# Kernel tuning notes

Hardware: AMD Instinct MI355X
Metric: run time of the kernel (lower is better)

## Reference

```python
import jax, jax.numpy as jnp
import numpy as np

N = 20000      # nodes
E = 160000     # edges
F_IN = 128     # num_node_features
D = 128        # embedding_size (out_channels)
H = 4          # heads
NEG = 0.2      # GATv2Conv negative_slope
N_LAYERS = 3


def setup_inputs() -> dict:
    key = jax.random.key(0)
    ks = jax.random.split(key, 12)
    s = 0.05
    return {
        "x": jax.random.normal(ks[0], (N, F_IN), jnp.float32),
        "edge_index": jax.random.randint(ks[1], (2, E), 0, N, jnp.int64),
        "edge_attr": jax.random.normal(ks[2], (E, 2), jnp.float32),
        "Wf": jax.random.normal(ks[3], (F_IN, D), jnp.float32) * s,
        "bf": jnp.zeros((D,), jnp.float32),
        "Wl": jax.random.normal(ks[4], (D, H * D), jnp.float32) * s,
        "bl": jnp.zeros((H * D,), jnp.float32),
        "Wr": jax.random.normal(ks[5], (D, H * D), jnp.float32) * s,
        "br": jnp.zeros((H * D,), jnp.float32),
        "We": jax.random.normal(ks[6], (2, H * D), jnp.float32) * s,
        "att": jax.random.normal(ks[7], (H, D), jnp.float32) * s,
        "bias_out": jnp.zeros((D,), jnp.float32),
    }


def reference(x, edge_index, edge_attr, Wf, bf, Wl, bl, Wr, br, We, att, bias_out):
    src, dst = edge_index[0], edge_index[1]

    # add_self_loops with fill_value='mean': self-loop edge_attr = mean of
    # incoming edge_attr per node (0 where a node has no incoming edges)
    ea_sum = jax.ops.segment_sum(edge_attr, dst, num_segments=N)            # [N,2]
    cnt = jax.ops.segment_sum(jnp.ones((E,), edge_attr.dtype), dst, num_segments=N)
    loop_attr = ea_sum / jnp.maximum(cnt, 1.0)[:, None]
    loop_idx = jnp.arange(N, dtype=src.dtype)
    fsrc = jnp.concatenate([src, loop_idx])                                  # [E+N]
    fdst = jnp.concatenate([dst, loop_idx])
    fea = jnp.concatenate([edge_attr, loop_attr], axis=0)                    # [E+N,2]

    ee = (fea @ We).reshape(-1, H, D)                                        # [E+N,H,D]

    def gatv2_layer(h):
        xl = (h @ Wl + bl).reshape(N, H, D)   # lin_l -> source-side / message
        xr = (h @ Wr + br).reshape(N, H, D)   # lin_r -> target-side
        e = jax.nn.leaky_relu(xl[fsrc] + xr[fdst] + ee, NEG)                 # [E+N,H,D]
        logits = jnp.einsum('ehd,hd->eh', e, att)                            # [E+N,H]
        m = jax.ops.segment_max(logits, fdst, num_segments=N)                # [N,H]
        w = jnp.exp(logits - m[fdst])
        denom = jax.ops.segment_sum(w, fdst, num_segments=N)                 # [N,H]
        alpha = w / denom[fdst]                                              # segment softmax
        msg = xl[fsrc] * alpha[..., None]                                    # [E+N,H,D]
        out = jax.ops.segment_sum(msg, fdst, num_segments=N)                 # [N,H,D]
        return out.mean(axis=1) + bias_out                                   # concat=False

    h = x @ Wf + bf
    for _ in range(N_LAYERS):
        h = jax.nn.leaky_relu(gatv2_layer(h), 0.01)  # F.leaky_relu default slope
    return h
```

## Files before the change

kernel.cpp:

```cpp
#include <hip/hip_runtime.h>
#include <hip/hip_bf16.h>

#define NN 20000
#define NE 160000
#define EF (NE + NN)
#define DD 128
#define HH 4
#define NPA (NN * DD)
#define NPW (1024 * 128 + 128 * 128 + 1024)
#define DEGB ((NE + 255) / 256)
#define NBLK 40

typedef unsigned short u16;
typedef unsigned int u32;

using short8  = __attribute__((ext_vector_type(8))) short;
using ushort8 = __attribute__((ext_vector_type(8))) unsigned short;
using float4v = __attribute__((ext_vector_type(4))) float;

__device__ __forceinline__ float bf2f(u16 u) {
    union { u32 i; float f; } c;
    c.i = ((u32)u) << 16;
    return c.f;
}
__device__ __forceinline__ u16 f2bf(float f) {
    union { float f; u32 u; } c;
    c.f = f;
    u32 u = c.u;
    u32 r = (u + 0x7fffu + ((u >> 16) & 1u)) >> 16;
    return (u16)r;
}


__global__ void k_zero_i(int* __restrict__ p, int n) {
    int i = blockIdx.x * blockDim.x + threadIdx.x;
    if (i < n) p[i] = 0;
}

__global__ void k_zero_f(float* __restrict__ p, int n) {
    int i = blockIdx.x * blockDim.x + threadIdx.x;
    if (i < n) p[i] = 0.f;
}


__global__ void k_degpack(const int* __restrict__ ei, const float* __restrict__ ea,
                          const float* __restrict__ x,
                          const float* __restrict__ Wl, const float* __restrict__ Wr,
                          const float* __restrict__ bl, const float* __restrict__ br,
                          const float* __restrict__ Wf,
                          int* __restrict__ cnt, float* __restrict__ ea_sum,
                          u16* __restrict__ Axh, u16* __restrict__ Axl,
                          u16* __restrict__ W2Th, u16* __restrict__ W2Tl,
                          u16* __restrict__ WfTh, u16* __restrict__ WfTl,
                          float* __restrict__ bias2) {
    int gb = blockIdx.x;
    if (gb < DEGB) {
        int e = gb * 256 + threadIdx.x;
        if (e >= NE) return;
        int t = ei[NE + e];
        atomicAdd(&cnt[t], 1);
        atomicAdd(&ea_sum[t * 2 + 0], ea[e * 2 + 0]);
        atomicAdd(&ea_sum[t * 2 + 1], ea[e * 2 + 1]);
        return;
    }
    int i = (gb - DEGB) * 256 + threadIdx.x;
    if (i < NPA) {
        float a = x[i];
        u16 h = f2bf(a);
        Axh[i] = h;
        Axl[i] = f2bf(a - bf2f(h));
        return;
    }
    i -= NPA;
    if (i < 1024 * 128) {
        int n = i >> 7, k = i & 127;
        float w = (n < 512) ? Wl[k * 512 + n] : Wr[k * 512 + (n - 512)];
        u16 h = f2bf(w);
        W2Th[n * 128 + k] = h;
        W2Tl[n * 128 + k] = f2bf(w - bf2f(h));
    } else if (i < 1024 * 128 + 128 * 128) {
        int u = i - 1024 * 128;
        int n = u >> 7, k = u & 127;
        float w = Wf[k * 128 + n];
        u16 h = f2bf(w);
        WfTh[n * 128 + k] = h;
        WfTl[n * 128 + k] = f2bf(w - bf2f(h));
    } else if (i < NPW) {
        int n = i - (1024 * 128 + 128 * 128);
        bias2[n] = (n < 512) ? bl[n] : br[n - 512];
    }
}


__global__ __launch_bounds__(512) void k_scan_a(const int* __restrict__ cnt,
                                                int* __restrict__ rowptr,
                                                int* __restrict__ bsum) {
    __shared__ int ws[8];
    int tid = threadIdx.x;
    int i = blockIdx.x * 512 + tid;
    int l = tid & 63, w = tid >> 6;
    int v = (i < NN) ? (cnt[i] + 1) : 0;
    #pragma unroll
    for (int off = 1; off < 64; off <<= 1) {
        int u = __shfl_up(v, off, 64);
        if (l >= off) v += u;
    }
    if (l == 63) ws[w] = v;
    __syncthreads();
    if (w == 0) {
        int s = (l < 8) ? ws[l] : 0;
        #pragma unroll
        for (int off = 1; off < 8; off <<= 1) {
            int u = __shfl_up(s, off, 64);
            if (l >= off) s += u;
        }
        if (l < 8) ws[l] = s;
    }
    __syncthreads();
    v += (w > 0) ? ws[w - 1] : 0;
    if (i < NN) rowptr[i + 1] = v;
    if (tid == 511) bsum[blockIdx.x] = v;
}

__global__ void k_scan_c(int* __restrict__ rowptr, const int* __restrict__ bsum) {
    int l = threadIdx.x & 63;
    int v = (l < NBLK) ? bsum[l] : 0;
    #pragma unroll
    for (int off = 1; off < 64; off <<= 1) {
        int u = __shfl_up(v, off, 64);
        if (l >= off) v += u;
    }
    int i = blockIdx.x * blockDim.x + threadIdx.x;
    int j = i >> 9;
    int off = (j > 0) ? __shfl(v, j - 1, 64) : 0;
    if (i < NN) rowptr[i + 1] += off;
    if (i == 0) rowptr[0] = 0;
}


__global__ void k_fill(const int* __restrict__ ei, const float* __restrict__ ea,
                       const int* __restrict__ rowptr, int* __restrict__ fillc,
                       const int* __restrict__ cnt, const float* __restrict__ ea_sum,
                       int* __restrict__ srcs,
                       float* __restrict__ fa0, float* __restrict__ fa1) {
    int e = blockIdx.x * blockDim.x + threadIdx.x;
    if (e < NE) {
        int s = ei[e], t = ei[NE + e];
        int pos = atomicAdd(&fillc[t], 1);
        int slot = rowptr[t] + pos;
        srcs[slot] = s;
        fa0[slot] = ea[e * 2];
        fa1[slot] = ea[e * 2 + 1];
    } else if (e < NE + NN) {
        int n = e - NE;
        int slot = rowptr[n + 1] - 1;
        srcs[slot] = n;
        float c = fmaxf((float)cnt[n], 1.f);
        fa0[slot] = ea_sum[n * 2 + 0] / c;
        fa1[slot] = ea_sum[n * 2 + 1] / c;
    }
}


template<int SPLIT, int NB>
__global__ __launch_bounds__(256, 3) void k_mgemm(
        const u16* __restrict__ Ahg, const u16* __restrict__ Alg,
        const u16* __restrict__ BTh, const u16* __restrict__ BTl,
        const float* __restrict__ bias, float* __restrict__ C1,
        u16* __restrict__ C2b,
        u16* __restrict__ Oh, u16* __restrict__ Ol, int M) {
    __shared__ u16 sAh[64 * 128], sBh[64 * 128], sBl[64 * 128];
    int m0 = blockIdx.y * 64;
    int t = threadIdx.x;
    int lane = t & 63;
    int wm = (t >> 6) & 1;
    int wn = t >> 7;
    int fm = lane & 15;
    int q8 = (lane >> 4) * 8;

    short8 fal[4][2];
    #pragma unroll
    for (int i = 0; i < 2; ++i) {
        const u16* p = Alg + (size_t)(m0 + wm * 32 + i * 16 + fm) * 128 + q8;
        #pragma unroll
        for (int kk = 0; kk < 4; ++kk)
            fal[kk][i] = *(const short8*)(p + kk * 32);
    }

    #pragma unroll
    for (int i = 0; i < 4; ++i) {
        int c = t + 256 * i;
        int row = c >> 4, ch = c & 15;
        int gm = m0 + row;
        short8 va = {0, 0, 0, 0, 0, 0, 0, 0};
        if (gm < M) va = *(const short8*)&Ahg[gm * 128 + ch * 8];
        *(short8*)&sAh[row * 128 + ((ch ^ (row & 15)) << 3)] = va;
    }

    int cq = q8 >> 3;

    for (int bb = 0; bb < NB; ++bb) {
        int n0 = (blockIdx.x * NB + bb) * 64;
        __syncthreads();
        #pragma unroll
        for (int i = 0; i < 4; ++i) {
            int c = t + 256 * i;
            int row = c >> 4, ch = c & 15;
            int gn = n0 + row;
            int d = row * 128 + ((ch ^ (row & 15)) << 3);
            *(short8*)&sBh[d] = *(const short8*)&BTh[gn * 128 + ch * 8];
            *(short8*)&sBl[d] = *(const short8*)&BTl[gn * 128 + ch * 8];
        }
        __syncthreads();

        float4v zz = {0.f, 0.f, 0.f, 0.f};
        float4v acc[2][2];
        acc[0][0] = zz; acc[0][1] = zz; acc[1][0] = zz; acc[1][1] = zz;

        #pragma unroll
        for (int k0 = 0; k0 < 128; k0 += 32) {
            int cl = (k0 >> 3) + cq;
            int sw = (cl ^ fm) << 3;
            short8 fah[2], fbh[2], fbl[2];
            #pragma unroll
            for (int i = 0; i < 2; ++i) {
                int mr = wm * 32 + i * 16 + fm;
                fah[i] = *(const short8*)&sAh[mr * 128 + sw];
                int nr = wn * 32 + i * 16 + fm;
                fbh[i] = *(const short8*)&sBh[nr * 128 + sw];
                fbl[i] = *(const short8*)&sBl[nr * 128 + sw];
            }
            #pragma unroll
            for (int i = 0; i < 2; ++i)
                #pragma unroll
                for (int j = 0; j < 2; ++j) {
                    acc[i][j] = __builtin_amdgcn_mfma_f32_16x16x32_bf16(fah[i], fbh[j], acc[i][j], 0, 0, 0);
                    acc[i][j] = __builtin_amdgcn_mfma_f32_16x16x32_bf16(fah[i], fbl[j], acc[i][j], 0, 0, 0);
                    acc[i][j] = __builtin_amdgcn_mfma_f32_16x16x32_bf16(fal[k0 >> 5][i], fbh[j], acc[i][j], 0, 0, 0);
                }
        }

        #pragma unroll
        for (int i = 0; i < 2; ++i) {
            #pragma unroll
            for (int j = 0; j < 2; ++j) {
                int gn = n0 + wn * 32 + j * 16 + fm;
                float bv = bias[gn];
                #pragma unroll
                for (int r = 0; r < 4; ++r) {
                    int gm = m0 + wm * 32 + i * 16 + (lane >> 4) * 4 + r;
                    if (gm < M) {
                        float v = acc[i][j][r] + bv;
                        if (SPLIT) {
                            u16 h = f2bf(v);
                            Oh[gm * 128 + gn] = h;
                            Ol[gm * 128 + gn] = f2bf(v - bf2f(h));
                        } else if (n0 < 512) {
                            C1[gm * 512 + gn] = v;
                        } else {
                            C2b[gm * 512 + gn - 512] = f2bf(v);
                        }
                    }
                }
            }
        }
    }
}


__global__ __launch_bounds__(256) void k_gat(
        const int* __restrict__ rowptr, const int* __restrict__ srcs,
        const float* __restrict__ fa0, const float* __restrict__ fa1,
        const float* __restrict__ xl, const u16* __restrict__ xr,
        const float* __restrict__ We, const float* __restrict__ att,
        const float* __restrict__ bias_out,
        u16* __restrict__ Oh, u16* __restrict__ Ol,
        float* __restrict__ outp, int last) {
    __shared__ float sacc[2][512];
    __shared__ float sden[2][4];
    int wv = threadIdx.x >> 6;
    int pair = wv >> 1;
    int half = wv & 1;
    int n = blockIdx.x * 2 + pair;
    int l = threadIdx.x & 63;
    int d0 = l * 8;
    float xrv[8], we0[8], we1[8], atv[8];
    {
        ushort8 u = *reinterpret_cast<const ushort8*>(&xr[(size_t)n * 512 + d0]);
        #pragma unroll
        for (int k = 0; k < 8; ++k) xrv[k] = bf2f(u[k]);
        float4 a = *reinterpret_cast<const float4*>(&We[d0]);
        float4 b = *reinterpret_cast<const float4*>(&We[d0 + 4]);
        we0[0]=a.x; we0[1]=a.y; we0[2]=a.z; we0[3]=a.w;
        we0[4]=b.x; we0[5]=b.y; we0[6]=b.z; we0[7]=b.w;
        a = *reinterpret_cast<const float4*>(&We[512 + d0]);
        b = *reinterpret_cast<const float4*>(&We[512 + d0 + 4]);
        we1[0]=a.x; we1[1]=a.y; we1[2]=a.z; we1[3]=a.w;
        we1[4]=b.x; we1[5]=b.y; we1[6]=b.z; we1[7]=b.w;
        a = *reinterpret_cast<const float4*>(&att[d0]);
        b = *reinterpret_cast<const float4*>(&att[d0 + 4]);
        atv[0]=a.x; atv[1]=a.y; atv[2]=a.z; atv[3]=a.w;
        atv[4]=b.x; atv[5]=b.y; atv[6]=b.z; atv[7]=b.w;
    }
    int b0 = rowptr[n], b1 = rowptr[n + 1];
    float acc[8] = {0.f,0.f,0.f,0.f,0.f,0.f,0.f,0.f};
    float den = 0.f;
    int e0 = b0 + half;
    if (e0 < b1) {
        int sNext = srcs[e0];
        for (int e = e0; e < b1; e += 2) {
            int s = sNext;
            if (e + 2 < b1) sNext = srcs[e + 2];
            float f0 = fa0[e], f1 = fa1[e];
            const float* xlp = &xl[(size_t)s * 512 + d0];
            float4 a = *reinterpret_cast<const float4*>(xlp);
            float4 b = *reinterpret_cast<const float4*>(xlp + 4);
            float xv[8] = {a.x, a.y, a.z, a.w, b.x, b.y, b.z, b.w};
            float p = 0.f;
            #pragma unroll
            for (int k = 0; k < 8; ++k) {
                float v = xv[k] + xrv[k] + f0 * we0[k] + f1 * we1[k];
                v = v > 0.f ? v : 0.2f * v;
                p += v * atv[k];
            }
            p += __shfl_xor(p, 1, 64);
            p += __shfl_xor(p, 2, 64);
            p += __shfl_xor(p, 4, 64);
            p += __shfl_xor(p, 8, 64);
            float wt = __expf(p);
            den += wt;
            #pragma unroll
            for (int k = 0; k < 8; ++k) acc[k] += wt * xv[k];
        }
    }
    if (half == 1) {
        *reinterpret_cast<float4*>(&sacc[pair][d0]) =
            make_float4(acc[0], acc[1], acc[2], acc[3]);
        *reinterpret_cast<float4*>(&sacc[pair][d0 + 4]) =
            make_float4(acc[4], acc[5], acc[6], acc[7]);
        if ((l & 15) == 0) sden[pair][l >> 4] = den;
    }
    __syncthreads();
    if (half == 1) return;
    #pragma unroll
    for (int k = 0; k < 8; ++k) acc[k] += sacc[pair][d0 + k];
    den += sden[pair][l >> 4];
    float inv = 1.f / den;
    float val[8];
    #pragma unroll
    for (int k = 0; k < 8; ++k) {
        float v = acc[k] * inv;
        v += __shfl_xor(v, 16, 64);
        v += __shfl_xor(v, 32, 64);
        val[k] = v;
    }
    if (l < 16) {
        #pragma unroll
        for (int k = 0; k < 8; ++k) {
            float v = val[k] * 0.25f + bias_out[d0 + k];
            v = v > 0.f ? v : 0.01f * v;
            val[k] = v;
        }
        if (last) {
            #pragma unroll
            for (int k = 0; k < 8; ++k) outp[n * 128 + d0 + k] = val[k];
        } else {
            #pragma unroll
            for (int k = 0; k < 8; ++k) {
                u16 hv = f2bf(val[k]);
                Oh[n * 128 + d0 + k] = hv;
                Ol[n * 128 + d0 + k] = f2bf(val[k] - bf2f(hv));
            }
        }
    }
}


extern "C" void kernel_launch(void* const* d_in, const int* in_sizes, int n_in,
                              void* d_out, int out_size, void* d_ws, size_t ws_size,
                              hipStream_t stream) {
    size_t o = 0;
    auto alloc = [&](size_t bytes) { size_t cur = o; o += (bytes + 255) & ~(size_t)255; return cur; };
    size_t off_cnt    = alloc((size_t)NN * 4);
    size_t off_fillc  = alloc((size_t)NN * 4);
    size_t off_easum  = alloc((size_t)NN * 2 * 4);
    size_t off_rowptr = alloc((size_t)(NN + 1) * 4);
    size_t off_bsum   = alloc((size_t)NBLK * 4);
    size_t off_srcs   = alloc((size_t)EF * 4);
    size_t off_fa0    = alloc((size_t)EF * 4);
    size_t off_fa1    = alloc((size_t)EF * 4);
    size_t off_axh    = alloc((size_t)NN * DD * 2);
    size_t off_axl    = alloc((size_t)NN * DD * 2);
    size_t off_ah     = alloc((size_t)NN * DD * 2);
    size_t off_al     = alloc((size_t)NN * DD * 2);
    size_t off_xl     = alloc((size_t)NN * 512 * 4);
    size_t off_xr     = alloc((size_t)NN * 512 * 2);
    size_t off_w2th   = alloc((size_t)1024 * 128 * 2);
    size_t off_w2tl   = alloc((size_t)1024 * 128 * 2);
    size_t off_wfth   = alloc((size_t)128 * 128 * 2);
    size_t off_wftl   = alloc((size_t)128 * 128 * 2);
    size_t off_bias2  = alloc((size_t)1024 * 4);
    size_t need = o;

    bool ok = (n_in == 12) && d_ws != nullptr && ws_size >= need
           && out_size == NN * DD
           && in_sizes[0] == NN * DD && in_sizes[1] == 2 * NE
           && in_sizes[2] == NE * 2 && in_sizes[3] == 128 * 128
           && in_sizes[5] == 128 * 512 && in_sizes[9] == 2 * 512
           && in_sizes[10] == 4 * 128 && in_sizes[11] == 128;
    if (!ok) {
        k_zero_f<<<(NN * DD + 255) / 256, 256, 0, stream>>>((float*)d_out, NN * DD);
        return;
    }

    const float* x        = (const float*)d_in[0];
    const int*   ei       = (const int*)d_in[1];
    const float* ea       = (const float*)d_in[2];
    const float* Wf       = (const float*)d_in[3];
    const float* bf       = (const float*)d_in[4];
    const float* Wl       = (const float*)d_in[5];
    const float* bl       = (const float*)d_in[6];
    const float* Wr       = (const float*)d_in[7];
    const float* br       = (const float*)d_in[8];
    const float* We       = (const float*)d_in[9];
    const float* att      = (const float*)d_in[10];
    const float* bias_out = (const float*)d_in[11];

    char* base = (char*)d_ws;
    int*   cnt    = (int*)(base + off_cnt);
    int*   fillc  = (int*)(base + off_fillc);
    float* ea_sum = (float*)(base + off_easum);
    int*   rowptr = (int*)(base + off_rowptr);
    int*   bsum   = (int*)(base + off_bsum);
    int*   srcs   = (int*)(base + off_srcs);
    float* fa0    = (float*)(base + off_fa0);
    float* fa1    = (float*)(base + off_fa1);
    u16*   Axh    = (u16*)(base + off_axh);
    u16*   Axl    = (u16*)(base + off_axl);
    u16*   Ah     = (u16*)(base + off_ah);
    u16*   Al     = (u16*)(base + off_al);
    float* xl     = (float*)(base + off_xl);
    u16*   xr     = (u16*)(base + off_xr);
    u16*   W2Th   = (u16*)(base + off_w2th);
    u16*   W2Tl   = (u16*)(base + off_w2tl);
    u16*   WfTh   = (u16*)(base + off_wfth);
    u16*   WfTl   = (u16*)(base + off_wftl);
    float* bias2  = (float*)(base + off_bias2);

    int zero_ints = (int)((off_easum + (size_t)NN * 2 * 4 - off_cnt) / 4);
    k_zero_i<<<(zero_ints + 255) / 256, 256, 0, stream>>>(cnt, zero_ints);

    int packb = (NPA + NPW + 255) / 256;
    k_degpack<<<DEGB + packb, 256, 0, stream>>>(ei, ea, x, Wl, Wr, bl, br, Wf,
                                                cnt, ea_sum, Axh, Axl,
                                                W2Th, W2Tl, WfTh, WfTl, bias2);
    k_scan_a<<<NBLK, 512, 0, stream>>>(cnt, rowptr, bsum);
    k_scan_c<<<(NN + 255) / 256, 256, 0, stream>>>(rowptr, bsum);
    k_fill<<<(NE + NN + 255) / 256, 256, 0, stream>>>(ei, ea, rowptr, fillc,
                                                      cnt, ea_sum, srcs, fa0, fa1);

    const int MT = (NN + 63) / 64;
    k_mgemm<1, 2><<<dim3(1, MT), 256, 0, stream>>>(Axh, Axl, WfTh, WfTl,
                                                   bf, nullptr, nullptr, Ah, Al, NN);

    for (int layer = 0; layer < 3; ++layer) {
        k_mgemm<0, 8><<<dim3(2, MT), 256, 0, stream>>>(Ah, Al, W2Th, W2Tl,
                                                       bias2, xl, xr, nullptr, nullptr, NN);
        int last = (layer == 2);
        k_gat<<<NN / 2, 256, 0, stream>>>(rowptr, srcs, fa0, fa1, xl, xr,
                                          We, att, bias_out, Ah, Al,
                                          (float*)d_out, last);
    }
}
```

Measured before the change: 413.0 us.

## Packed-FMA leaky-relu, DPP reductions, and wave-wide edge metadata preload in GAT kernel

Rewrites the GAT aggregation inner loop to use packed two-wide float FMAs. Leaky-relu followed by the attention dot becomes 0.6*v + 0.4*|v|, which removes the compare and select. The cross-lane logit reduction uses DPP adds instead of shuffles. Edge source indices and attributes for up to 64 edges are loaded once per wave and broadcast with readlane, with a slow fallback loop for nodes of higher degree. This cuts dependent global loads and ALU work per edge, at the cost of more code complexity and a loop bound that depends on degree.

```diff
diff --git a/kernel.cpp b/kernel.cpp
--- a/kernel.cpp
+++ b/kernel.cpp
@@ -17,6 +17,7 @@
 using short8  = __attribute__((ext_vector_type(8))) short;
 using ushort8 = __attribute__((ext_vector_type(8))) unsigned short;
 using float4v = __attribute__((ext_vector_type(4))) float;
+using f32x2   = __attribute__((ext_vector_type(2))) float;
 
 __device__ __forceinline__ float bf2f(u16 u) {
     union { u32 i; float f; } c;
@@ -29,6 +30,13 @@
     u32 u = c.u;
     u32 r = (u + 0x7fffu + ((u >> 16) & 1u)) >> 16;
     return (u16)r;
+}
+
+template<int CTRL>
+__device__ __forceinline__ float dpp_add(float v) {
+    int t = __builtin_amdgcn_update_dpp(0, __builtin_bit_cast(int, v),
+                                        CTRL, 0xf, 0xf, true);
+    return v + __builtin_bit_cast(float, t);
 }
 
 
@@ -284,64 +292,107 @@
     int n = blockIdx.x * 2 + pair;
     int l = threadIdx.x & 63;
     int d0 = l * 8;
-    float xrv[8], we0[8], we1[8], atv[8];
+
+    f32x2 xr2[4], we0p[4], we1p[4], at6p[4], at4p[4];
     {
         ushort8 u = *reinterpret_cast<const ushort8*>(&xr[(size_t)n * 512 + d0]);
         #pragma unroll
-        for (int k = 0; k < 8; ++k) xrv[k] = bf2f(u[k]);
-        float4 a = *reinterpret_cast<const float4*>(&We[d0]);
-        float4 b = *reinterpret_cast<const float4*>(&We[d0 + 4]);
-        we0[0]=a.x; we0[1]=a.y; we0[2]=a.z; we0[3]=a.w;
-        we0[4]=b.x; we0[5]=b.y; we0[6]=b.z; we0[7]=b.w;
-        a = *reinterpret_cast<const float4*>(&We[512 + d0]);
-        b = *reinterpret_cast<const float4*>(&We[512 + d0 + 4]);
-        we1[0]=a.x; we1[1]=a.y; we1[2]=a.z; we1[3]=a.w;
-        we1[4]=b.x; we1[5]=b.y; we1[6]=b.z; we1[7]=b.w;
-        a = *reinterpret_cast<const float4*>(&att[d0]);
-        b = *reinterpret_cast<const float4*>(&att[d0 + 4]);
-        atv[0]=a.x; atv[1]=a.y; atv[2]=a.z; atv[3]=a.w;
-        atv[4]=b.x; atv[5]=b.y; atv[6]=b.z; atv[7]=b.w;
-    }
+        for (int k = 0; k < 4; ++k) {
+            f32x2 t; t.x = bf2f(u[2 * k]); t.y = bf2f(u[2 * k + 1]);
+            xr2[k] = t;
+        }
+        const f32x2* w0 = reinterpret_cast<const f32x2*>(&We[d0]);
+        const f32x2* w1 = reinterpret_cast<const f32x2*>(&We[512 + d0]);
+        const f32x2* av = reinterpret_cast<const f32x2*>(&att[d0]);
+        #pragma unroll
+        for (int k = 0; k < 4; ++k) {
+            we0p[k] = w0[k];
+            we1p[k] = w1[k];
+            f32x2 a = av[k];
+            at6p[k] = a * 0.6f;
+            at4p[k] = a * 0.4f;
+        }
+    }
+
     int b0 = rowptr[n], b1 = rowptr[n + 1];
-    float acc[8] = {0.f,0.f,0.f,0.f,0.f,0.f,0.f,0.f};
+    int nit = (b1 - b0 - half + 1) >> 1;
+
+    int sv = 0, f0i = 0, f1i = 0;
+    {
+        int me = b0 + half + 2 * l;
+        if (l < nit) {
+            sv  = srcs[me];
+            f0i = __builtin_bit_cast(int, fa0[me]);
+            f1i = __builtin_bit_cast(int, fa1[me]);
+        }
+    }
+
+    f32x2 acc2[4];
+    acc2[0] = f32x2{0.f, 0.f}; acc2[1] = f32x2{0.f, 0.f};
+    acc2[2] = f32x2{0.f, 0.f}; acc2[3] = f32x2{0.f, 0.f};
     float den = 0.f;
-    int e0 = b0 + half;
-    if (e0 < b1) {
-        int sNext = srcs[e0];
-        for (int e = e0; e < b1; e += 2) {
-            int s = sNext;
-            if (e + 2 < b1) sNext = srcs[e + 2];
-            float f0 = fa0[e], f1 = fa1[e];
-            const float* xlp = &xl[(size_t)s * 512 + d0];
-            float4 a = *reinterpret_cast<const float4*>(xlp);
-            float4 b = *reinterpret_cast<const float4*>(xlp + 4);
-            float xv[8] = {a.x, a.y, a.z, a.w, b.x, b.y, b.z, b.w};
-            float p = 0.f;
-            #pragma unroll
-            for (int k = 0; k < 8; ++k) {
-                float v = xv[k] + xrv[k] + f0 * we0[k] + f1 * we1[k];
-                v = v > 0.f ? v : 0.2f * v;
-                p += v * atv[k];
-            }
-            p += __shfl_xor(p, 1, 64);
-            p += __shfl_xor(p, 2, 64);
-            p += __shfl_xor(p, 4, 64);
-            p += __shfl_xor(p, 8, 64);
-            float wt = __expf(p);
-            den += wt;
-            #pragma unroll
-            for (int k = 0; k < 8; ++k) acc[k] += wt * xv[k];
-        }
-    }
+
+    auto body = [&](float4 A, float4 B, float f0, float f1) {
+        f32x2 f0p; f0p.x = f0; f0p.y = f0;
+        f32x2 f1p; f1p.x = f1; f1p.y = f1;
+        f32x2 xv2[4];
+        xv2[0].x = A.x; xv2[0].y = A.y;
+        xv2[1].x = A.z; xv2[1].y = A.w;
+        xv2[2].x = B.x; xv2[2].y = B.y;
+        xv2[3].x = B.z; xv2[3].y = B.w;
+        f32x2 p2 = {0.f, 0.f};
+        #pragma unroll
+        for (int k = 0; k < 4; ++k) {
+            f32x2 t = __builtin_elementwise_fma(f0p, we0p[k], xr2[k]);
+            t = __builtin_elementwise_fma(f1p, we1p[k], t);
+            f32x2 v2 = xv2[k] + t;
+            f32x2 a2 = __builtin_elementwise_abs(v2);
+            p2 = __builtin_elementwise_fma(at6p[k], v2, p2);
+            p2 = __builtin_elementwise_fma(at4p[k], a2, p2);
+        }
+        float p = p2.x + p2.y;
+        p = dpp_add<0xB1>(p);
+        p = dpp_add<0x4E>(p);
+        p = dpp_add<0x124>(p);
+        p = dpp_add<0x128>(p);
+        float wt = __expf(p);
+        den += wt;
+        f32x2 wtp; wtp.x = wt; wtp.y = wt;
+        #pragma unroll
+        for (int k = 0; k < 4; ++k)
+            acc2[k] = __builtin_elementwise_fma(wtp, xv2[k], acc2[k]);
+    };
+
+    int nfast = nit < 64 ? nit : 64;
+    #pragma unroll 2
+    for (int it = 0; it < nfast; ++it) {
+        int   s  = __builtin_amdgcn_readlane(sv, it);
+        float f0 = __builtin_bit_cast(float, __builtin_amdgcn_readlane(f0i, it));
+        float f1 = __builtin_bit_cast(float, __builtin_amdgcn_readlane(f1i, it));
+        const float* xp = &xl[(size_t)s * 512 + d0];
+        float4 A = *reinterpret_cast<const float4*>(xp);
+        float4 B = *reinterpret_cast<const float4*>(xp + 4);
+        body(A, B, f0, f1);
+    }
+    for (int e = b0 + half + 128; e < b1; e += 2) {
+        int s = srcs[e];
+        const float* xp = &xl[(size_t)s * 512 + d0];
+        float4 A = *reinterpret_cast<const float4*>(xp);
+        float4 B = *reinterpret_cast<const float4*>(xp + 4);
+        body(A, B, fa0[e], fa1[e]);
+    }
+
     if (half == 1) {
         *reinterpret_cast<float4*>(&sacc[pair][d0]) =
-            make_float4(acc[0], acc[1], acc[2], acc[3]);
+            make_float4(acc2[0].x, acc2[0].y, acc2[1].x, acc2[1].y);
         *reinterpret_cast<float4*>(&sacc[pair][d0 + 4]) =
-            make_float4(acc[4], acc[5], acc[6], acc[7]);
+            make_float4(acc2[2].x, acc2[2].y, acc2[3].x, acc2[3].y);
         if ((l & 15) == 0) sden[pair][l >> 4] = den;
     }
     __syncthreads();
     if (half == 1) return;
+    float acc[8] = {acc2[0].x, acc2[0].y, acc2[1].x, acc2[1].y,
+                    acc2[2].x, acc2[2].y, acc2[3].x, acc2[3].y};
     #pragma unroll
     for (int k = 0; k < 8; ++k) acc[k] += sacc[pair][d0 + k];
     den += sden[pair][l >> 4];
```

New measurement: 405.3 us. No clear change (-1.9%).
